# Kernel optimization log

Measured on AMD Instinct MI355X. Metric: run time of the kernel, lower is better.

The kernel has to match this reference:

```python
import jax, jax.numpy as jnp
import numpy as np

B, L, D, H = 4, 1024, 768, 12
HD = D // H  # head_dim = 64
SCALING = HD ** -0.5


def setup_inputs() -> dict:
    key = jax.random.key(0)
    ks = jax.random.split(key, 6)
    x = jax.random.normal(ks[0], (B, L, D), dtype=jnp.float32)
    attn_bias = jax.random.normal(ks[1], (B, H, L, L), dtype=jnp.float32)
    s_in = 1.0 / np.sqrt(D)
    w_in = jax.random.uniform(ks[2], (3 * D, D), dtype=jnp.float32, minval=-s_in, maxval=s_in)
    b_in = jax.random.uniform(ks[3], (3 * D,), dtype=jnp.float32, minval=-s_in, maxval=s_in)
    w_out = jax.random.uniform(ks[4], (D, D), dtype=jnp.float32, minval=-s_in, maxval=s_in)
    b_out = jax.random.uniform(ks[5], (D,), dtype=jnp.float32, minval=-s_in, maxval=s_in)
    return {"x": x, "attn_bias": attn_bias, "w_in": w_in, "b_in": b_in,
            "w_out": w_out, "b_out": b_out}


def reference(x, attn_bias, w_in, b_in, w_out, b_out):
    # fused QKV projection: [B, L, 3D]
    qkv = jnp.einsum('bld,ed->ble', x, w_in) + b_in
    q, k, v = jnp.split(qkv, 3, axis=-1)
    # [B, H, L, HD]
    q = q.reshape(B, L, H, HD).transpose(0, 2, 1, 3) * SCALING
    k = k.reshape(B, L, H, HD).transpose(0, 2, 1, 3)
    v = v.reshape(B, L, H, HD).transpose(0, 2, 1, 3)
    # bias-augmented attention scores: [B, H, L, L]
    scores = jnp.einsum('bhqd,bhkd->bhqk', q, k) + attn_bias
    probs = jax.nn.softmax(scores, axis=-1)
    # attend: [B, H, L, HD] -> [B, L, D]
    o = jnp.einsum('bhqk,bhkd->bhqd', probs, v)
    o = o.transpose(0, 2, 1, 3).reshape(B, L, D)
    return jnp.einsum('bld,ed->ble', o, w_out) + b_out
```

## Files before the change

kernel.cpp:

```cpp
#include <hip/hip_runtime.h>
#include <hip/hip_bf16.h>
#include <stdint.h>

#define B_ 4
#define L_ 1024
#define D_ 768
#define H_ 12
#define HD_ 64
#define M_ 4096
#define N3_ 2304

typedef float f32x4 __attribute__((ext_vector_type(4)));
typedef float f32x4v __attribute__((ext_vector_type(4)));
typedef short bf16x8 __attribute__((ext_vector_type(8)));
typedef unsigned short u16;
typedef u16 u16x8 __attribute__((ext_vector_type(8)));
typedef u16 u16x4 __attribute__((ext_vector_type(4)));
typedef uint32_t u32x2 __attribute__((ext_vector_type(2)));

#define AS3 __attribute__((address_space(3)))
#define AS1 __attribute__((address_space(1)))

__device__ __forceinline__ void gll16(const void* g, void* l) {
  __builtin_amdgcn_global_load_lds((const AS1 void*)g, (AS3 void*)l, 16, 0, 0);
}

__device__ __forceinline__ u16 f2bf(float f) {
  uint32_t u = __builtin_bit_cast(uint32_t, f);
  u += 0x7fffu + ((u >> 16) & 1u);
  return (u16)(u >> 16);
}

__global__ void k_cvt3(const float* __restrict__ a, u16* __restrict__ ao, int na4,
                       const float* __restrict__ b, u16* __restrict__ bo, int nb4,
                       const float* __restrict__ c, u16* __restrict__ co, int nc4) {
  int i = blockIdx.x * 256 + threadIdx.x;
  const float* src;
  u16* dst;
  if (i < na4) {
    src = a; dst = ao;
  } else if (i < na4 + nb4) {
    src = b; dst = bo; i -= na4;
  } else if (i < na4 + nb4 + nc4) {
    src = c; dst = co; i -= na4 + nb4;
  } else {
    return;
  }
  f32x4v v = ((const f32x4v*)src)[i];
  u16x4 o;
  o.x = f2bf(v.x); o.y = f2bf(v.y); o.z = f2bf(v.z); o.w = f2bf(v.w);
  ((u16x4*)dst)[i] = o;
}

__global__ __launch_bounds__(256) void k_gemm_qkv(
    const u16* __restrict__ Xb, const u16* __restrict__ Wb,
    const float* __restrict__ b_in,
    u16* __restrict__ gQ, u16* __restrict__ gK, u16* __restrict__ gV) {
  __shared__ u16 As[128 * 64];
  __shared__ u16 Bs[128 * 64];
  const int tid = threadIdx.x;
  const int lane = tid & 63;
  const int w = tid >> 6;
  const int wm = (w >> 1) * 64;
  const int wn = (w & 1) * 64;
  const int lr = lane & 15;
  const int lg = lane >> 4;
  const int m0 = blockIdx.x * 128;
  const int n0 = blockIdx.y * 128;

  f32x4 acc[4][4];
#pragma unroll
  for (int i = 0; i < 4; ++i)
#pragma unroll
    for (int j = 0; j < 4; ++j) acc[i][j] = (f32x4){0.f, 0.f, 0.f, 0.f};

  for (int kt = 0; kt < 12; ++kt) {
    __syncthreads();
#pragma unroll
    for (int i = 0; i < 4; ++i) {
      int seg = i * 256 + tid;
      int row = seg >> 3;
      int sl = (seg & 7) ^ (row & 7);
      gll16(Xb + (size_t)(m0 + row) * 768 + kt * 64 + sl * 8, (char*)As + seg * 16);
      gll16(Wb + (size_t)(n0 + row) * 768 + kt * 64 + sl * 8, (char*)Bs + seg * 16);
    }
    __syncthreads();
#pragma unroll
    for (int kh = 0; kh < 2; ++kh) {
      bf16x8 af[4], bfr[4];
#pragma unroll
      for (int t = 0; t < 4; ++t) {
        int ra = wm + t * 16 + lr;
        af[t] = *(const bf16x8*)((const char*)As + ra * 128 +
                                 ((kh * 64 + lg * 16) ^ ((ra & 7) << 4)));
        int rb = wn + t * 16 + lr;
        bfr[t] = *(const bf16x8*)((const char*)Bs + rb * 128 +
                                  ((kh * 64 + lg * 16) ^ ((rb & 7) << 4)));
      }
#pragma unroll
      for (int mi = 0; mi < 4; ++mi)
#pragma unroll
        for (int ni = 0; ni < 4; ++ni)
          acc[mi][ni] = __builtin_amdgcn_mfma_f32_16x16x32_bf16(
              af[mi], bfr[ni], acc[mi][ni], 0, 0, 0);
    }
  }
  const int sec = blockIdx.y / 6;
  u16* dst = sec == 0 ? gQ : (sec == 1 ? gK : gV);
  const float scale = sec == 0 ? 0.125f : 1.0f;
#pragma unroll
  for (int ni = 0; ni < 4; ++ni) {
    int e = n0 + wn + ni * 16 + lr;
    float bias = b_in[e];
    int es = e - sec * 768;
    int h = es >> 6, d = es & 63;
#pragma unroll
    for (int mi = 0; mi < 4; ++mi) {
#pragma unroll
      for (int j = 0; j < 4; ++j) {
        int m = m0 + wm + mi * 16 + lg * 4 + j;
        int bb = m >> 10, lq = m & 1023;
        float vv = (acc[mi][ni][j] + bias) * scale;
        dst[(size_t)((bb * 12 + h) * 1024 + lq) * 64 + d] = f2bf(vv);
      }
    }
  }
}

__global__ __launch_bounds__(256) void k_transpose(const u16* __restrict__ V,
                                                   u16* __restrict__ Vt) {
  __shared__ u16 t[64][66];
  const int tid = threadIdx.x;
  const int bh = blockIdx.x >> 4;
  const int kv0 = (blockIdx.x & 15) * 64;
  {
    int r = tid >> 2, c0 = (tid & 3) * 16;
    const u16* src = V + (size_t)(bh * 1024 + kv0 + r) * 64 + c0;
#pragma unroll
    for (int p = 0; p < 2; ++p) {
      u16x8 x = *(const u16x8*)(src + p * 8);
#pragma unroll
      for (int e = 0; e < 8; ++e) t[r][c0 + p * 8 + e] = x[e];
    }
  }
  __syncthreads();
  {
    int d = tid >> 2, k0 = (tid & 3) * 16;
    u16* dst = Vt + (size_t)(bh * 64 + d) * 1024 + kv0 + k0;
#pragma unroll
    for (int p = 0; p < 2; ++p) {
      u16x8 o;
#pragma unroll
      for (int e = 0; e < 8; ++e) o[e] = t[k0 + p * 8 + e][d];
      *(u16x8*)(dst + p * 8) = o;
    }
  }
}

__global__ __launch_bounds__(256) void k_attn(
    const u16* __restrict__ gQ, const u16* __restrict__ gK,
    const u16* __restrict__ gVt, const float* __restrict__ gBias,
    u16* __restrict__ gO) {
  __shared__ u16 Ks[2][64 * 64];
  __shared__ u16 Vs[2][64 * 64];
  __shared__ f32x4 PlV[4][256];
  const int tid = threadIdx.x;
  const int lane = tid & 63;
  const int w = tid >> 6;
  const int lr = lane & 15;
  const int lg = lane >> 4;
  const int lb = (blockIdx.x & 7) * 48 + (blockIdx.x >> 3);
  const int bh = lb >> 3;
  const int q0 = (lb & 7) * 128;
  const int qr0 = q0 + w * 16;
  const int qr1 = q0 + 64 + w * 16;

#define STAGE_KV(buf, kv0)                                                     \
  do {                                                                         \
    _Pragma("unroll") for (int i_ = 0; i_ < 2; ++i_) {                         \
      int seg_ = i_ * 256 + tid;                                               \
      int row_ = seg_ >> 3;                                                    \
      int sl_ = (seg_ & 7) ^ (row_ & 7);                                       \
      gll16(gK + (size_t)(bh * 1024 + (kv0) + row_) * 64 + sl_ * 8,            \
            (char*)Ks[buf] + seg_ * 16);                                       \
      gll16(gVt + (size_t)(bh * 64 + row_) * 1024 + (kv0) + sl_ * 8,           \
            (char*)Vs[buf] + seg_ * 16);                                       \
    }                                                                          \
  } while (0)

  const float* bline0 = gBias + (size_t)(bh * 1024 + qr0 + lr) * 1024;
  const float* bline1 = gBias + (size_t)(bh * 1024 + qr1 + lr) * 1024;

  bf16x8 qa[2][2];
#pragma unroll
  for (int kh = 0; kh < 2; ++kh) {
    qa[0][kh] = *(const bf16x8*)(gQ + (size_t)(bh * 1024 + qr0 + lr) * 64 + kh * 32 + lg * 8);
    qa[1][kh] = *(const bf16x8*)(gQ + (size_t)(bh * 1024 + qr1 + lr) * 64 + kh * 32 + lg * 8);
  }

  f32x4 oacc[2][4];
#pragma unroll
  for (int p = 0; p < 2; ++p)
#pragma unroll
    for (int dt = 0; dt < 4; ++dt) oacc[p][dt] = (f32x4){0.f, 0.f, 0.f, 0.f};
  float mrow[2] = {-1e30f, -1e30f}, lrow[2] = {0.f, 0.f};

  char* plw = (char*)PlV[w];
  const int swz = (lr & 7) << 4;

  STAGE_KV(0, 0);
  f32x4 bcur[2][4];
#pragma unroll
  for (int ni = 0; ni < 4; ++ni) {
    bcur[0][ni] = *(const f32x4*)(bline0 + ni * 16 + lg * 4);
    bcur[1][ni] = *(const f32x4*)(bline1 + ni * 16 + lg * 4);
  }
  __syncthreads();

  for (int t = 0; t < 16; ++t) {
    const int cur = t & 1;
    const int kv0 = t * 64;
    if (t < 15) STAGE_KV(cur ^ 1, kv0 + 64);

    f32x4 s[2][4];
#pragma unroll
    for (int p = 0; p < 2; ++p)
#pragma unroll
      for (int ni = 0; ni < 4; ++ni) s[p][ni] = (f32x4){0.f, 0.f, 0.f, 0.f};
    __builtin_amdgcn_s_setprio(1);
#pragma unroll
    for (int kh = 0; kh < 2; ++kh)
#pragma unroll
      for (int ni = 0; ni < 4; ++ni) {
        int rk = ni * 16 + lr;
        bf16x8 kb = *(const bf16x8*)((const char*)Ks[cur] + rk * 128 +
                                     ((kh * 64 + lg * 16) ^ ((rk & 7) << 4)));
        s[0][ni] = __builtin_amdgcn_mfma_f32_16x16x32_bf16(kb, qa[0][kh], s[0][ni], 0, 0, 0);
        s[1][ni] = __builtin_amdgcn_mfma_f32_16x16x32_bf16(kb, qa[1][kh], s[1][ni], 0, 0, 0);
      }
    __builtin_amdgcn_s_setprio(0);

#pragma unroll
    for (int ni = 0; ni < 4; ++ni) {
      s[0][ni] += bcur[0][ni];
      s[1][ni] += bcur[1][ni];
    }
    if (t < 15) {
#pragma unroll
      for (int ni = 0; ni < 4; ++ni) {
        bcur[0][ni] = *(const f32x4*)(bline0 + kv0 + 64 + ni * 16 + lg * 4);
        bcur[1][ni] = *(const f32x4*)(bline1 + kv0 + 64 + ni * 16 + lg * 4);
      }
    }

#pragma unroll
    for (int p = 0; p < 2; ++p) {
      float mx0 = fmaxf(fmaxf(s[p][0][0], s[p][0][1]), fmaxf(s[p][0][2], s[p][0][3]));
      float mx1 = fmaxf(fmaxf(s[p][1][0], s[p][1][1]), fmaxf(s[p][1][2], s[p][1][3]));
      float mx2 = fmaxf(fmaxf(s[p][2][0], s[p][2][1]), fmaxf(s[p][2][2], s[p][2][3]));
      float mx3 = fmaxf(fmaxf(s[p][3][0], s[p][3][1]), fmaxf(s[p][3][2], s[p][3][3]));
      float vmax = fmaxf(fmaxf(mx0, mx1), fmaxf(mx2, mx3));
      vmax = fmaxf(vmax, __shfl_xor(vmax, 16));
      vmax = fmaxf(vmax, __shfl_xor(vmax, 32));
      float mnew = fmaxf(mrow[p], vmax);
      float al = __expf(mrow[p] - mnew);
      mrow[p] = mnew;
#pragma unroll
      for (int ni = 0; ni < 4; ++ni)
#pragma unroll
        for (int j = 0; j < 4; ++j) s[p][ni][j] = __expf(s[p][ni][j] - mnew);
      float r0 = (s[p][0][0] + s[p][0][1]) + (s[p][0][2] + s[p][0][3]);
      float r1 = (s[p][1][0] + s[p][1][1]) + (s[p][1][2] + s[p][1][3]);
      float r2 = (s[p][2][0] + s[p][2][1]) + (s[p][2][2] + s[p][2][3]);
      float r3 = (s[p][3][0] + s[p][3][1]) + (s[p][3][2] + s[p][3][3]);
      float rs = (r0 + r1) + (r2 + r3);
      rs += __shfl_xor(rs, 16);
      rs += __shfl_xor(rs, 32);
      lrow[p] = lrow[p] * al + rs;
      f32x4 av;
#pragma unroll
      for (int j = 0; j < 4; ++j) av[j] = __shfl(al, (lane & 48) | (lg * 4 + j));
#pragma unroll
      for (int dt = 0; dt < 4; ++dt) oacc[p][dt] *= av;
    }

#pragma unroll
    for (int p = 0; p < 2; ++p) {
      char* pl = plw + p * 2048;
#pragma unroll
      for (int ni = 0; ni < 4; ++ni) {
        uint32_t w0 = (uint32_t)f2bf(s[p][ni][0]) | ((uint32_t)f2bf(s[p][ni][1]) << 16);
        uint32_t w1 = (uint32_t)f2bf(s[p][ni][2]) | ((uint32_t)f2bf(s[p][ni][3]) << 16);
        u32x2 pv = {w0, w1};
        *(u32x2*)(pl + lr * 128 + ((ni * 32 + lg * 8) ^ swz)) = pv;
      }
    }
    __builtin_amdgcn_s_setprio(1);
#pragma unroll
    for (int kh = 0; kh < 2; ++kh) {
      bf16x8 pa0 = *(const bf16x8*)(plw + lr * 128 + ((kh * 64 + lg * 16) ^ swz));
      bf16x8 pa1 = *(const bf16x8*)(plw + 2048 + lr * 128 + ((kh * 64 + lg * 16) ^ swz));
#pragma unroll
      for (int dt = 0; dt < 4; ++dt) {
        int rv = dt * 16 + lr;
        bf16x8 vb = *(const bf16x8*)((const char*)Vs[cur] + rv * 128 +
                                     ((kh * 64 + lg * 16) ^ ((rv & 7) << 4)));
        oacc[0][dt] = __builtin_amdgcn_mfma_f32_16x16x32_bf16(pa0, vb, oacc[0][dt], 0, 0, 0);
        oacc[1][dt] = __builtin_amdgcn_mfma_f32_16x16x32_bf16(pa1, vb, oacc[1][dt], 0, 0, 0);
      }
    }
    __builtin_amdgcn_s_setprio(0);

    __syncthreads();
  }

  const int bg = bh / 12, h = bh % 12;
#pragma unroll
  for (int p = 0; p < 2; ++p) {
    float inv = 1.0f / lrow[p];
    f32x4 iv;
#pragma unroll
    for (int j = 0; j < 4; ++j) iv[j] = __shfl(inv, (lane & 48) | (lg * 4 + j));
    const int qrp = p == 0 ? qr0 : qr1;
#pragma unroll
    for (int j = 0; j < 4; ++j) {
      int row = qrp + lg * 4 + j;
#pragma unroll
      for (int dt = 0; dt < 4; ++dt) {
        gO[(size_t)(bg * 1024 + row) * 768 + h * 64 + dt * 16 + lr] =
            f2bf(oacc[p][dt][j] * iv[j]);
      }
    }
  }
#undef STAGE_KV
}

__global__ __launch_bounds__(256) void k_gemm_out(
    const u16* __restrict__ Ob, const u16* __restrict__ Wb,
    const float* __restrict__ b_out, float* __restrict__ out) {
  __shared__ u16 As[64 * 64];
  __shared__ u16 Bs[64 * 64];
  const int tid = threadIdx.x;
  const int lane = tid & 63;
  const int w = tid >> 6;
  const int wm = (w >> 1) * 32;
  const int wn = (w & 1) * 32;
  const int lr = lane & 15;
  const int lg = lane >> 4;
  const int m0 = blockIdx.x * 64;
  const int n0 = blockIdx.y * 64;

  f32x4 acc[2][2];
#pragma unroll
  for (int i = 0; i < 2; ++i)
#pragma unroll
    for (int j = 0; j < 2; ++j) acc[i][j] = (f32x4){0.f, 0.f, 0.f, 0.f};

  for (int kt = 0; kt < 12; ++kt) {
    __syncthreads();
#pragma unroll
    for (int i = 0; i < 2; ++i) {
      int seg = i * 256 + tid;
      int row = seg >> 3;
      int sl = (seg & 7) ^ (row & 7);
      gll16(Ob + (size_t)(m0 + row) * 768 + kt * 64 + sl * 8, (char*)As + seg * 16);
      gll16(Wb + (size_t)(n0 + row) * 768 + kt * 64 + sl * 8, (char*)Bs + seg * 16);
    }
    __syncthreads();
#pragma unroll
    for (int kh = 0; kh < 2; ++kh) {
      bf16x8 af[2], bfr[2];
#pragma unroll
      for (int t = 0; t < 2; ++t) {
        int ra = wm + t * 16 + lr;
        af[t] = *(const bf16x8*)((const char*)As + ra * 128 +
                                 ((kh * 64 + lg * 16) ^ ((ra & 7) << 4)));
        int rb = wn + t * 16 + lr;
        bfr[t] = *(const bf16x8*)((const char*)Bs + rb * 128 +
                                  ((kh * 64 + lg * 16) ^ ((rb & 7) << 4)));
      }
#pragma unroll
      for (int mi = 0; mi < 2; ++mi)
#pragma unroll
        for (int ni = 0; ni < 2; ++ni)
          acc[mi][ni] = __builtin_amdgcn_mfma_f32_16x16x32_bf16(
              af[mi], bfr[ni], acc[mi][ni], 0, 0, 0);
    }
  }
#pragma unroll
  for (int ni = 0; ni < 2; ++ni) {
    int n = n0 + wn + ni * 16 + lr;
    float bias = b_out[n];
#pragma unroll
    for (int mi = 0; mi < 2; ++mi) {
#pragma unroll
      for (int j = 0; j < 4; ++j) {
        int m = m0 + wm + mi * 16 + lg * 4 + j;
        out[(size_t)m * 768 + n] = acc[mi][ni][j] + bias;
      }
    }
  }
}

extern "C" void kernel_launch(void* const* d_in, const int* in_sizes, int n_in,
                              void* d_out, int out_size, void* d_ws, size_t ws_size,
                              hipStream_t stream) {
  const float* x = (const float*)d_in[0];
  const float* attn_bias = (const float*)d_in[1];
  const float* w_in = (const float*)d_in[2];
  const float* b_in = (const float*)d_in[3];
  const float* w_out = (const float*)d_in[4];
  const float* b_out = (const float*)d_in[5];
  float* out = (float*)d_out;

  char* ws = (char*)d_ws;
  size_t off = 0;
  u16* xb = (u16*)(ws + off);  off += (size_t)M_ * D_ * 2;
  u16* wib = (u16*)(ws + off); off += (size_t)N3_ * D_ * 2;
  u16* wob = (u16*)(ws + off); off += (size_t)D_ * D_ * 2;
  u16* q = (u16*)(ws + off);   off += (size_t)48 * 1024 * 64 * 2;
  u16* k = (u16*)(ws + off);   off += (size_t)48 * 1024 * 64 * 2;
  u16* v = (u16*)(ws + off);   off += (size_t)48 * 1024 * 64 * 2;
  u16* vt = (u16*)(ws + off);  off += (size_t)48 * 1024 * 64 * 2;
  u16* ob = (u16*)(ws + off);  off += (size_t)M_ * D_ * 2;

  const int na4 = (M_ * D_) / 4;
  const int nb4 = (N3_ * D_) / 4;
  const int nc4 = (D_ * D_) / 4;
  k_cvt3<<<(na4 + nb4 + nc4 + 255) / 256, 256, 0, stream>>>(
      x, xb, na4, w_in, wib, nb4, w_out, wob, nc4);
  k_gemm_qkv<<<dim3(32, 18), 256, 0, stream>>>(xb, wib, b_in, q, k, v);
  k_transpose<<<768, 256, 0, stream>>>(v, vt);
  k_attn<<<384, 256, 0, stream>>>(q, k, vt, attn_bias, ob);
  k_gemm_out<<<dim3(64, 12), 256, 0, stream>>>(ob, wob, b_out, out);
}
```

Before: 115.8 us.

## Deepen attention K/V pipeline to four LDS stages and double-buffer bias loads

The attention kernel now keeps four K/V shared-memory buffers and processes two KV tiles per loop iteration, prefetching the next two tiles and the next bias chunks while computing. This halves the number of block-wide barriers and gives global loads more time to land. In exchange LDS use roughly doubles to about 40KB per block and register pressure rises from the extra bias buffer. A launch bound requesting two blocks per CU is added to cap registers, which may cause spills.

After: 114.3 us. Within noise of the previous version (-1.3%).

```diff
diff --git a/kernel.cpp b/kernel.cpp
--- a/kernel.cpp
+++ b/kernel.cpp
@@ -157,12 +157,12 @@
   }
 }
 
-__global__ __launch_bounds__(256) void k_attn(
+__global__ __launch_bounds__(256, 2) void k_attn(
     const u16* __restrict__ gQ, const u16* __restrict__ gK,
     const u16* __restrict__ gVt, const float* __restrict__ gBias,
     u16* __restrict__ gO) {
-  __shared__ u16 Ks[2][64 * 64];
-  __shared__ u16 Vs[2][64 * 64];
+  __shared__ u16 Ks[4][64 * 64];
+  __shared__ u16 Vs[4][64 * 64];
   __shared__ f32x4 PlV[4][256];
   const int tid = threadIdx.x;
   const int lane = tid & 63;
@@ -191,6 +191,14 @@
   const float* bline0 = gBias + (size_t)(bh * 1024 + qr0 + lr) * 1024;
   const float* bline1 = gBias + (size_t)(bh * 1024 + qr1 + lr) * 1024;
 
+#define BIAS_LOAD(dst, kv0)                                                    \
+  do {                                                                         \
+    _Pragma("unroll") for (int ni_ = 0; ni_ < 4; ++ni_) {                      \
+      dst[0][ni_] = *(const f32x4*)(bline0 + (kv0) + ni_ * 16 + lg * 4);       \
+      dst[1][ni_] = *(const f32x4*)(bline1 + (kv0) + ni_ * 16 + lg * 4);       \
+    }                                                                          \
+  } while (0)
+
   bf16x8 qa[2][2];
 #pragma unroll
   for (int kh = 0; kh < 2; ++kh) {
@@ -208,20 +216,9 @@
   char* plw = (char*)PlV[w];
   const int swz = (lr & 7) << 4;
 
-  STAGE_KV(0, 0);
-  f32x4 bcur[2][4];
-#pragma unroll
-  for (int ni = 0; ni < 4; ++ni) {
-    bcur[0][ni] = *(const f32x4*)(bline0 + ni * 16 + lg * 4);
-    bcur[1][ni] = *(const f32x4*)(bline1 + ni * 16 + lg * 4);
-  }
-  __syncthreads();
-
-  for (int t = 0; t < 16; ++t) {
-    const int cur = t & 1;
-    const int kv0 = t * 64;
-    if (t < 15) STAGE_KV(cur ^ 1, kv0 + 64);
-
+  f32x4 b0[2][4], b1[2][4];
+
+  auto tile_body = [&](int cur, f32x4 (&bc)[2][4]) {
     f32x4 s[2][4];
 #pragma unroll
     for (int p = 0; p < 2; ++p)
@@ -242,15 +239,8 @@
 
 #pragma unroll
     for (int ni = 0; ni < 4; ++ni) {
-      s[0][ni] += bcur[0][ni];
-      s[1][ni] += bcur[1][ni];
-    }
-    if (t < 15) {
-#pragma unroll
-      for (int ni = 0; ni < 4; ++ni) {
-        bcur[0][ni] = *(const f32x4*)(bline0 + kv0 + 64 + ni * 16 + lg * 4);
-        bcur[1][ni] = *(const f32x4*)(bline1 + kv0 + 64 + ni * 16 + lg * 4);
-      }
+      s[0][ni] += bc[0][ni];
+      s[1][ni] += bc[1][ni];
     }
 
 #pragma unroll
@@ -310,8 +300,27 @@
       }
     }
     __builtin_amdgcn_s_setprio(0);
-
-    __syncthreads();
+  };
+
+  STAGE_KV(0, 0);
+  STAGE_KV(1, 64);
+  BIAS_LOAD(b0, 0);
+  BIAS_LOAD(b1, 64);
+  __syncthreads();
+
+  for (int i = 0; i < 8; ++i) {
+    const int t0 = 2 * i;
+    if (i < 7) {
+      STAGE_KV((t0 + 2) & 3, (t0 + 2) * 64);
+      STAGE_KV((t0 + 3) & 3, (t0 + 3) * 64);
+    }
+    tile_body(t0 & 3, b0);
+    if (i < 7) BIAS_LOAD(b0, (t0 + 2) * 64);
+    tile_body((t0 + 1) & 3, b1);
+    if (i < 7) {
+      BIAS_LOAD(b1, (t0 + 3) * 64);
+      __syncthreads();
+    }
   }
 
   const int bg = bh / 12, h = bh % 12;
@@ -333,6 +342,7 @@
     }
   }
 #undef STAGE_KV
+#undef BIAS_LOAD
 }
 
 __global__ __launch_bounds__(256) void k_gemm_out(
```
